# Kernel tuning notes

Hardware: AMD Instinct MI355X
Metric: run time of the kernel (lower is better)

The kernel has to match this reference:

```python
import jax, jax.numpy as jnp
import numpy as np
from jax import lax

ALPHA = float(np.exp(-1.0 / 5.0))   # exp(-1/tau_mem), tau_mem=5.0
THRESHOLD = 1.0


def _dwconv(x, w, b, groups):
    # x: (B, Cin, T), w: (Cout, Cin/groups, K), 'same' padding for odd K
    pad = (w.shape[-1] - 1) // 2
    y = lax.conv_general_dilated(
        x, w, window_strides=(1,), padding=[(pad, pad)],
        dimension_numbers=("NCH", "OIH", "NCH"), feature_group_count=groups)
    return y + b[None, :, None]


def setup_inputs() -> dict:
    key = jax.random.key(0)
    ks = jax.random.split(key, 12)
    B, C, T = 8, 256, 4096
    OP = 6            # out_per_kernel for each of the 3 kernel sizes
    DEC = 128         # decoder_channels
    f32 = jnp.float32
    d = {}
    d["x"] = jax.random.normal(ks[0], (B, C, T), f32)
    # depthwise multi-path conv params (groups=C): weight (C*OP, 1, K)
    d["w3"] = jax.random.normal(ks[1], (C * OP, 1, 3), f32) * 0.2
    d["b3"] = jnp.zeros((C * OP,), f32)
    d["w5"] = jax.random.normal(ks[2], (C * OP, 1, 5), f32) * 0.15
    d["b5"] = jnp.zeros((C * OP,), f32)
    d["w9"] = jax.random.normal(ks[3], (C * OP, 1, 9), f32) * 0.1
    d["b9"] = jnp.zeros((C * OP,), f32)
    # reduce: Conv1d(C*18 -> C, k=1, groups=C): weight (C, 18, 1)
    d["w_red"] = jax.random.normal(ks[4], (C, 3 * OP, 1), f32) * 0.2
    d["b_red"] = jnp.zeros((C,), f32)
    d["latency_scale"] = jnp.asarray(5.0, f32)
    # output_gates: xavier uniform (C, C) with zero diagonal
    bound = float(np.sqrt(6.0 / (C + C)))
    og = jax.random.uniform(ks[5], (C, C), f32, -bound, bound)
    d["output_gates"] = og * (1.0 - jnp.eye(C, dtype=f32))
    d["bias"] = jnp.zeros((C,), f32)
    # post_mlp: Linear(C, DEC) -> ReLU -> Linear(DEC, C); stored as (in, out)
    d["W1"] = jax.random.normal(ks[6], (C, DEC), f32) * float(np.sqrt(2.0 / C))
    d["b1"] = jnp.zeros((DEC,), f32)
    d["W2"] = jax.random.normal(ks[7], (DEC, C), f32) * float(np.sqrt(2.0 / DEC))
    d["b2"] = jnp.zeros((C,), f32)
    return d


def reference(x, w3, b3, w5, b5, w9, b9, w_red, b_red,
              latency_scale, output_gates, bias, W1, b1, W2, b2):
    B, C, T = x.shape
    # DepthwiseMultiPathEncoder: 3 depthwise convs -> cat -> grouped 1x1 reduce
    o3 = _dwconv(x, w3, b3, C)
    o5 = _dwconv(x, w5, b5, C)
    o9 = _dwconv(x, w9, b9, C)
    cat = jnp.concatenate([o3, o5, o9], axis=1)      # (B, 18C, T)
    drive = _dwconv(cat, w_red, b_red, C)             # (B, C, T)
    # LIF membrane recurrence + first-spike latency (sequential over T)
    d_t = jnp.moveaxis(drive, 2, 0)                   # (T, B, C)
    def step(V, dt):
        V = ALPHA * V + (1.0 - ALPHA) * dt
        return V, V >= THRESHOLD
    _, crossed = lax.scan(step, jnp.zeros((B, C), x.dtype), d_t)  # (T, B, C) bool
    fired_any = crossed.any(axis=0)
    first_t = jnp.argmax(crossed, axis=0)             # first True index
    true_latency = jnp.where(fired_any, first_t, T).astype(x.dtype)  # (B, C)
    # latency -> activation -> gated mix -> MLP -> softplus, clamp [0, T]
    scale = jnp.maximum(latency_scale, 0.001)
    act = jnp.exp(-true_latency / scale)              # (B, C)
    mixed = act @ output_gates.T + bias[None, :]      # (B, C)
    h = jax.nn.relu(mixed @ W1 + b1)
    raw_pred = h @ W2 + b2
    pred_latency = jnp.clip(jax.nn.softplus(raw_pred), 0.0, float(T))
    return pred_latency, true_latency, act
```

## Files before the change

### kernel.cpp

```cpp
#include <hip/hip_runtime.h>
#include <math.h>

#define C_CH 256
#define T_LEN 4096


__global__ __launch_bounds__(256, 2) void drive_scan_kernel(
    const float* __restrict__ x,
    const float* __restrict__ w3, const float* __restrict__ b3,
    const float* __restrict__ w5, const float* __restrict__ b5,
    const float* __restrict__ w9, const float* __restrict__ b9,
    const float* __restrict__ w_red, const float* __restrict__ b_red,
    const float* __restrict__ latency_scale,
    float* __restrict__ out_lat, float* __restrict__ out_act)
{
    const int blk  = blockIdx.x;
    const int b    = blk >> 8;
    const int c    = blk & 255;
    const int tid  = threadIdx.x;
    const int lane = tid & 63;
    const int wv   = tid >> 6;

    __shared__ float sWF[28];
    __shared__ float sHalo[3][8][256];
    __shared__ float sWaveTot[4];
    __shared__ float sCarry[4];
    __shared__ int   sMin[4];

    if (tid < 27) {
        const int r = tid / 9, k = tid - 9 * r;
        const int q0     = 18 * c + 6 * r;
        const int region = (q0 >= 1536) + (q0 >= 3072);
        const int p0     = q0 - region * 1536;
        const int K      = (region == 0) ? 3 : (region == 1 ? 5 : 9);
        const int off    = (9 - K) >> 1;
        const float* wP  = (region == 0) ? w3 : (region == 1 ? w5 : w9);
        const int kk     = k - off;
        float w = 0.0f;
        if (kk >= 0 && kk < K) {
            const float* wr = w_red + c * 18 + 6 * r;
            #pragma unroll
            for (int j = 0; j < 6; ++j)
                w = fmaf(wr[j], wP[(p0 + j) * K + kk], w);
        }
        sWF[tid] = w;
    } else if (tid == 27) {
        float acc = b_red[c];
        #pragma unroll
        for (int r = 0; r < 3; ++r) {
            const int q0     = 18 * c + 6 * r;
            const int region = (q0 >= 1536) + (q0 >= 3072);
            const int p0     = q0 - region * 1536;
            const float* bP  = (region == 0) ? b3 : (region == 1 ? b5 : b9);
            const float* wr  = w_red + c * 18 + 6 * r;
            #pragma unroll
            for (int j = 0; j < 6; ++j) acc = fmaf(wr[j], bP[p0 + j], acc);
        }
        sWF[27] = acc;
    }

    const int t0 = tid << 4;
    float d[16];
    #pragma unroll
    for (int r = 0; r < 3; ++r) {
        const int src = (3 * c + r) & 255;
        const float4* p = (const float4*)(x + ((size_t)b * C_CH + src) * T_LEN + t0);
        float xa[24];
        #pragma unroll
        for (int v = 0; v < 4; ++v) {
            float4 q = p[v];
            xa[4 + 4 * v + 0] = q.x; xa[4 + 4 * v + 1] = q.y;
            xa[4 + 4 * v + 2] = q.z; xa[4 + 4 * v + 3] = q.w;
        }
        #pragma unroll
        for (int k = 0; k < 4; ++k) {
            sHalo[r][k][tid]     = xa[4 + k];
            sHalo[r][4 + k][tid] = xa[16 + k];
        }
        __syncthreads();
        if (r == 0) {
            const float Beff = sWF[27];
            #pragma unroll
            for (int tt = 0; tt < 16; ++tt) d[tt] = Beff;
        }
        #pragma unroll
        for (int e = 0; e < 4; ++e)
            xa[e] = tid ? sHalo[r][4 + e][tid - 1] : 0.0f;
        #pragma unroll
        for (int e = 0; e < 4; ++e)
            xa[20 + e] = (tid < 255) ? sHalo[r][e][tid + 1] : 0.0f;
        #pragma unroll
        for (int k = 0; k < 9; ++k) {
            const float wk = sWF[r * 9 + k];
            #pragma unroll
            for (int tt = 0; tt < 16; ++tt)
                d[tt] = fmaf(wk, xa[tt + k], d[tt]);
        }
    }

    const float A   = (float)0.8187307530779818;
    const float OMA = (float)(1.0 - 0.8187307530779818);

    float S = 0.0f;
    #pragma unroll
    for (int tt = 0; tt < 16; ++tt) S = A * S + OMA * d[tt];

    const float Fp[6] = {
        (float)4.0762203978366215e-02,
        (float)1.6615572731739337e-03,
        (float)2.7607725720371943e-06,
        (float)7.6218649302532563e-12,
        (float)5.8092835977683129e-23,
        (float)3.3744728758705166e-45
    };
    float cinc = S;
    #pragma unroll
    for (int s = 0; s < 6; ++s) {
        const int o = 1 << s;
        const float y = __shfl_up(cinc, o, 64);
        if (lane >= o) cinc = fmaf(Fp[s], y, cinc);
    }
    if (lane == 63) sWaveTot[wv] = cinc;
    __syncthreads();
    if (tid == 0) {
        float g = 0.0f;
        #pragma unroll
        for (int w = 0; w < 4; ++w) { sCarry[w] = g; g = sWaveTot[w]; }
    }
    __syncthreads();
    const float cprev = __shfl_up(cinc, 1, 64);
    const float Vin = (lane ? cprev : 0.0f)
                    + expf(-3.2f * (float)lane) * sCarry[wv];

    float V = Vin;
    int firstT = T_LEN;
    #pragma unroll
    for (int tt = 0; tt < 16; ++tt) {
        V = A * V + OMA * d[tt];
        if (V >= 1.0f && firstT == T_LEN) firstT = t0 + tt;
    }

    #pragma unroll
    for (int o = 32; o > 0; o >>= 1)
        firstT = min(firstT, __shfl_xor(firstT, o, 64));
    if (lane == 0) sMin[wv] = firstT;
    __syncthreads();
    if (tid == 0) {
        const int f = min(min(sMin[0], sMin[1]), min(sMin[2], sMin[3]));
        const float lat   = (float)f;
        const float scale = fmaxf(latency_scale[0], 0.001f);
        out_lat[blk] = lat;
        out_act[blk] = expf(-lat / scale);
    }
}

__global__ __launch_bounds__(256) void mlp_kernel(
    const float* __restrict__ act,
    const float* __restrict__ og, const float* __restrict__ bias,
    const float* __restrict__ W1, const float* __restrict__ b1,
    const float* __restrict__ W2, const float* __restrict__ b2,
    float* __restrict__ out_pred)
{
    const int b = blockIdx.x;
    const int j = threadIdx.x;
    __shared__ float sAct[256];
    __shared__ float sOg[32][257];
    __shared__ float sMix[256];
    __shared__ float sH[128];

    sAct[j] = act[b * 256 + j];

    float mix = bias[j];
    for (int i0 = 0; i0 < 256; i0 += 32) {
        __syncthreads();
        #pragma unroll
        for (int m = 0; m < 32; ++m) {
            const int f  = (m << 8) + j;
            const int jj = f >> 5;
            const int ii = f & 31;
            sOg[ii][jj] = og[jj * 256 + i0 + ii];
        }
        __syncthreads();
        #pragma unroll
        for (int ii = 0; ii < 32; ++ii)
            mix = fmaf(sAct[i0 + ii], sOg[ii][j], mix);
    }
    sMix[j] = mix;
    __syncthreads();

    if (j < 128) {
        float h = b1[j];
        #pragma unroll 8
        for (int i = 0; i < 256; ++i) h = fmaf(sMix[i], W1[i * 128 + j], h);
        sH[j] = fmaxf(h, 0.0f);
    }
    __syncthreads();

    float raw = b2[j];
    #pragma unroll 8
    for (int k = 0; k < 128; ++k) raw = fmaf(sH[k], W2[k * 256 + j], raw);

    const float sp = fmaxf(raw, 0.0f) + log1pf(expf(-fabsf(raw)));
    out_pred[b * 256 + j] = fminf(fmaxf(sp, 0.0f), 4096.0f);
}

extern "C" void kernel_launch(void* const* d_in, const int* in_sizes, int n_in,
                              void* d_out, int out_size, void* d_ws, size_t ws_size,
                              hipStream_t stream) {
    const float* x    = (const float*)d_in[0];
    const float* w3   = (const float*)d_in[1];
    const float* b3   = (const float*)d_in[2];
    const float* w5   = (const float*)d_in[3];
    const float* b5   = (const float*)d_in[4];
    const float* w9   = (const float*)d_in[5];
    const float* b9   = (const float*)d_in[6];
    const float* wred = (const float*)d_in[7];
    const float* bred = (const float*)d_in[8];
    const float* ls   = (const float*)d_in[9];
    const float* og   = (const float*)d_in[10];
    const float* bias = (const float*)d_in[11];
    const float* W1   = (const float*)d_in[12];
    const float* b1   = (const float*)d_in[13];
    const float* W2   = (const float*)d_in[14];
    const float* b2   = (const float*)d_in[15];

    float* out      = (float*)d_out;
    float* out_pred = out;
    float* out_lat  = out + 2048;
    float* out_act  = out + 4096;

    drive_scan_kernel<<<2048, 256, 0, stream>>>(
        x, w3, b3, w5, b5, w9, b9, wred, bred, ls, out_lat, out_act);
    mlp_kernel<<<8, 256, 0, stream>>>(out_act, og, bias, W1, b1, W2, b2, out_pred);
}
```

Measured before the change: 137.4 us.

## Widen scan blocks to 512 threads and prefetch MLP weights into cache

Doubles the threads per block so each thread handles 8 timesteps instead of 16, double-buffers the halo shared memory, and reworks the cross-wave carry combine for 8 waves. It also adds 8 extra blocks that read the gate and MLP weight matrices into a workspace sink, to warm the cache before the MLP kernel runs. MLP loop unrolling goes from 8 to 32. The prefetch blocks do throwaway work, and the larger block shape changes register pressure and occupancy.

Measured after the change: 130.5 us. -5.0%, faster.

```diff
diff --git a/kernel.cpp b/kernel.cpp
--- a/kernel.cpp
+++ b/kernel.cpp
@@ -5,27 +5,52 @@
 #define T_LEN 4096
 
 
-__global__ __launch_bounds__(256, 2) void drive_scan_kernel(
+__global__ __launch_bounds__(512, 8) void drive_scan_kernel(
     const float* __restrict__ x,
     const float* __restrict__ w3, const float* __restrict__ b3,
     const float* __restrict__ w5, const float* __restrict__ b5,
     const float* __restrict__ w9, const float* __restrict__ b9,
     const float* __restrict__ w_red, const float* __restrict__ b_red,
     const float* __restrict__ latency_scale,
+    const float* __restrict__ og, const float* __restrict__ W1,
+    const float* __restrict__ W2, float* __restrict__ sink,
     float* __restrict__ out_lat, float* __restrict__ out_act)
 {
-    const int blk  = blockIdx.x;
+    const int blk = blockIdx.x;
+    const int tid = threadIdx.x;
+
+    if (blk >= 2048) {
+        const int id = (blk - 2048) * 512 + tid;
+        float acc = 0.0f;
+        const float4* og4 = (const float4*)og;
+        const float4* W14 = (const float4*)W1;
+        const float4* W24 = (const float4*)W2;
+        #pragma unroll
+        for (int v = 0; v < 4; ++v) {
+            float4 q = og4[id + v * 4096]; acc += q.x + q.y + q.z + q.w;
+        }
+        #pragma unroll
+        for (int v = 0; v < 2; ++v) {
+            float4 q = W14[id + v * 4096]; acc += q.x + q.y + q.z + q.w;
+        }
+        #pragma unroll
+        for (int v = 0; v < 2; ++v) {
+            float4 q = W24[id + v * 4096]; acc += q.x + q.y + q.z + q.w;
+        }
+        sink[id] = acc;
+        return;
+    }
+
     const int b    = blk >> 8;
     const int c    = blk & 255;
-    const int tid  = threadIdx.x;
     const int lane = tid & 63;
     const int wv   = tid >> 6;
 
     __shared__ float sWF[28];
-    __shared__ float sHalo[3][8][256];
-    __shared__ float sWaveTot[4];
-    __shared__ float sCarry[4];
-    __shared__ int   sMin[4];
+    __shared__ float sHalo[2][8][512];
+    __shared__ float sWaveTot[8];
+    __shared__ float sCarry[8];
+    __shared__ int   sMin[8];
 
     if (tid < 27) {
         const int r = tid / 9, k = tid - 9 * r;
@@ -59,41 +84,39 @@
         sWF[27] = acc;
     }
 
-    const int t0 = tid << 4;
-    float d[16];
+    const int t0 = tid << 3;
+    float d[8];
+    float Beff;
     #pragma unroll
     for (int r = 0; r < 3; ++r) {
+        const int buf = r & 1;
         const int src = (3 * c + r) & 255;
         const float4* p = (const float4*)(x + ((size_t)b * C_CH + src) * T_LEN + t0);
-        float xa[24];
-        #pragma unroll
-        for (int v = 0; v < 4; ++v) {
-            float4 q = p[v];
-            xa[4 + 4 * v + 0] = q.x; xa[4 + 4 * v + 1] = q.y;
-            xa[4 + 4 * v + 2] = q.z; xa[4 + 4 * v + 3] = q.w;
-        }
-        #pragma unroll
-        for (int k = 0; k < 4; ++k) {
-            sHalo[r][k][tid]     = xa[4 + k];
-            sHalo[r][4 + k][tid] = xa[16 + k];
-        }
+        float xa[16];
+        {
+            float4 q0 = p[0], q1 = p[1];
+            xa[4] = q0.x; xa[5] = q0.y; xa[6]  = q0.z; xa[7]  = q0.w;
+            xa[8] = q1.x; xa[9] = q1.y; xa[10] = q1.z; xa[11] = q1.w;
+        }
+        #pragma unroll
+        for (int e = 0; e < 8; ++e) sHalo[buf][e][tid] = xa[4 + e];
         __syncthreads();
         if (r == 0) {
-            const float Beff = sWF[27];
-            #pragma unroll
-            for (int tt = 0; tt < 16; ++tt) d[tt] = Beff;
+            Beff = sWF[27];
+            #pragma unroll
+            for (int tt = 0; tt < 8; ++tt) d[tt] = Beff;
         }
         #pragma unroll
         for (int e = 0; e < 4; ++e)
-            xa[e] = tid ? sHalo[r][4 + e][tid - 1] : 0.0f;
+            xa[e] = tid ? sHalo[buf][4 + e][tid - 1] : 0.0f;
         #pragma unroll
         for (int e = 0; e < 4; ++e)
-            xa[20 + e] = (tid < 255) ? sHalo[r][e][tid + 1] : 0.0f;
+            xa[12 + e] = (tid < 511) ? sHalo[buf][e][tid + 1] : 0.0f;
         #pragma unroll
         for (int k = 0; k < 9; ++k) {
             const float wk = sWF[r * 9 + k];
             #pragma unroll
-            for (int tt = 0; tt < 16; ++tt)
+            for (int tt = 0; tt < 8; ++tt)
                 d[tt] = fmaf(wk, xa[tt + k], d[tt]);
         }
     }
@@ -103,15 +126,15 @@
 
     float S = 0.0f;
     #pragma unroll
-    for (int tt = 0; tt < 16; ++tt) S = A * S + OMA * d[tt];
+    for (int tt = 0; tt < 8; ++tt) S = A * S + OMA * d[tt];
 
     const float Fp[6] = {
+        (float)2.0189651799465541e-01,
         (float)4.0762203978366215e-02,
         (float)1.6615572731739337e-03,
         (float)2.7607725720371943e-06,
         (float)7.6218649302532563e-12,
-        (float)5.8092835977683129e-23,
-        (float)3.3744728758705166e-45
+        (float)5.8092835977683129e-23
     };
     float cinc = S;
     #pragma unroll
@@ -123,19 +146,20 @@
     if (lane == 63) sWaveTot[wv] = cinc;
     __syncthreads();
     if (tid == 0) {
+        const float A512 = 3.3744728758705166e-45f;
         float g = 0.0f;
         #pragma unroll
-        for (int w = 0; w < 4; ++w) { sCarry[w] = g; g = sWaveTot[w]; }
+        for (int w = 0; w < 8; ++w) { sCarry[w] = g; g = sWaveTot[w] + A512 * g; }
     }
     __syncthreads();
     const float cprev = __shfl_up(cinc, 1, 64);
     const float Vin = (lane ? cprev : 0.0f)
-                    + expf(-3.2f * (float)lane) * sCarry[wv];
+                    + expf(-1.6f * (float)lane) * sCarry[wv];
 
     float V = Vin;
     int firstT = T_LEN;
     #pragma unroll
-    for (int tt = 0; tt < 16; ++tt) {
+    for (int tt = 0; tt < 8; ++tt) {
         V = A * V + OMA * d[tt];
         if (V >= 1.0f && firstT == T_LEN) firstT = t0 + tt;
     }
@@ -146,7 +170,9 @@
     if (lane == 0) sMin[wv] = firstT;
     __syncthreads();
     if (tid == 0) {
-        const int f = min(min(sMin[0], sMin[1]), min(sMin[2], sMin[3]));
+        int f = sMin[0];
+        #pragma unroll
+        for (int w = 1; w < 8; ++w) f = min(f, sMin[w]);
         const float lat   = (float)f;
         const float scale = fmaxf(latency_scale[0], 0.001f);
         out_lat[blk] = lat;
@@ -190,14 +216,14 @@
 
     if (j < 128) {
         float h = b1[j];
-        #pragma unroll 8
+        #pragma unroll 32
         for (int i = 0; i < 256; ++i) h = fmaf(sMix[i], W1[i * 128 + j], h);
         sH[j] = fmaxf(h, 0.0f);
     }
     __syncthreads();
 
     float raw = b2[j];
-    #pragma unroll 8
+    #pragma unroll 32
     for (int k = 0; k < 128; ++k) raw = fmaf(sH[k], W2[k * 256 + j], raw);
 
     const float sp = fmaxf(raw, 0.0f) + log1pf(expf(-fabsf(raw)));
@@ -224,12 +250,14 @@
     const float* W2   = (const float*)d_in[14];
     const float* b2   = (const float*)d_in[15];
 
+    float* sink     = (float*)d_ws;
     float* out      = (float*)d_out;
     float* out_pred = out;
     float* out_lat  = out + 2048;
     float* out_act  = out + 4096;
 
-    drive_scan_kernel<<<2048, 256, 0, stream>>>(
-        x, w3, b3, w5, b5, w9, b9, wred, bred, ls, out_lat, out_act);
+    drive_scan_kernel<<<2056, 512, 0, stream>>>(
+        x, w3, b3, w5, b5, w9, b9, wred, bred, ls,
+        og, W1, W2, sink, out_lat, out_act);
     mlp_kernel<<<8, 256, 0, stream>>>(out_act, og, bias, W1, b1, W2, b2, out_pred);
 }
```
